# Performance work log

Hardware: AMD Instinct MI355X
Metric: run time of the kernel (lower is better)

Reference implementation:

```python
import jax, jax.numpy as jnp
import numpy as np

K = 8  # knn_k
EPS = 1e-5


def _grid_edges(H, W):
    # 4-connectivity grid edges, both directions. Returns (src, tgt) numpy int arrays.
    idx = np.arange(H * W).reshape(H, W)
    right_a, right_b = idx[:, :-1].ravel(), idx[:, 1:].ravel()
    down_a, down_b = idx[:-1, :].ravel(), idx[1:, :].ravel()
    src = np.concatenate([right_a, right_b, down_a, down_b])
    tgt = np.concatenate([right_b, right_a, down_b, down_a])
    return src.astype(np.int32), tgt.astype(np.int32)


def setup_inputs() -> dict:
    key = jax.random.key(0)
    k1, _ = jax.random.split(key)
    feature_map = jax.random.normal(k1, (16, 256, 48, 48), dtype=jnp.float32)
    gamma = jnp.ones((256,), jnp.float32)
    beta = jnp.zeros((256,), jnp.float32)
    return {"feature_map": feature_map, "gamma": gamma, "beta": beta}


def reference(feature_map, gamma, beta):
    B, C, H, W = feature_map.shape
    N = H * W
    # flatten_feature_map: [B,C,H,W] -> [B,N,C]
    nodes = feature_map.reshape(B, C, N).transpose(0, 2, 1)

    # static grid edges (4-connectivity)
    g_src_np, g_tgt_np = _grid_edges(H, W)
    g_src = jnp.asarray(g_src_np)
    g_tgt = jnp.asarray(g_tgt_np)

    # feature-space kNN per sample (cdist + topk); exclude self with large diag
    big_diag = jnp.eye(N, dtype=nodes.dtype) * 1e9

    def knn_idx(x):  # x: [N, C]
        sq = jnp.sum(x * x, axis=1)
        d2 = sq[:, None] + sq[None, :] - 2.0 * (x @ x.T) + big_diag
        _, idx = jax.lax.top_k(-d2, K)  # [N, K] nearest neighbors
        return idx

    knn_src = jax.vmap(knn_idx)(nodes).reshape(B, N * K)  # per-sample sources
    knn_tgt = jnp.repeat(jnp.arange(N, dtype=jnp.int32), K)  # static targets

    tgt_all = jnp.concatenate([g_tgt, knn_tgt])  # same for all samples
    n_edges = tgt_all.shape[0]
    ones = jnp.ones((n_edges,), nodes.dtype)

    def aggregate(x, k_src):  # mean over incoming edges (fallback path)
        src_all = jnp.concatenate([g_src, k_src.astype(jnp.int32)])
        agg = jax.ops.segment_sum(x[src_all], tgt_all, num_segments=N)
        cnt = jax.ops.segment_sum(ones, tgt_all, num_segments=N)
        return agg / jnp.clip(cnt, 1.0)[:, None]

    refined = jax.vmap(aggregate)(nodes, knn_src)  # [B, N, C]

    # residual + LayerNorm over channel dim
    y = refined + nodes
    mu = jnp.mean(y, axis=-1, keepdims=True)
    var = jnp.mean((y - mu) ** 2, axis=-1, keepdims=True)
    y = (y - mu) * jax.lax.rsqrt(var + EPS) * gamma + beta

    # unflatten: [B,N,C] -> [B,C,H,W]
    return y.transpose(0, 2, 1).reshape(B, C, H, W)
```

## Files before the change

### kernel.cpp

```cpp
#include <hip/hip_runtime.h>

#define B_   16
#define C_   256
#define H_   48
#define W_   48
#define N_   (H_ * W_)
#define KNN  8

#define NG   (N_ / 32)
#define NT   17
#define FRAG 512
#define MPRE 10
#define JSPLIT 2
#define NCAND (JSPLIT * MPRE)

typedef __attribute__((ext_vector_type(8)))  short bf16x8;
typedef __attribute__((ext_vector_type(8)))  unsigned short u16x8;
typedef __attribute__((ext_vector_type(16))) float f32x16;

__device__ __forceinline__ unsigned short f2bf(float f) {
    unsigned int u = __float_as_uint(f);
    u = (u + 0x7FFF + ((u >> 16) & 1)) >> 16;
    return (unsigned short)u;
}
__device__ __forceinline__ float bf2f(unsigned short h) {
    return __uint_as_float(((unsigned int)h) << 16);
}
__device__ __forceinline__ bool lex_lt(float v, int i, float bv, int bi) {
    return (v < bv) || (v == bv && i < bi);
}
__device__ __forceinline__ unsigned int f2sort(float f) {
    unsigned int u = __float_as_uint(f);
    return u ^ ((unsigned int)((int)u >> 31) | 0x80000000u);
}

__global__ __launch_bounds__(256) void k_transpose(const float* __restrict__ fm,
                                                   float* __restrict__ nodes,
                                                   unsigned short* __restrict__ Xf) {
    __shared__ float tile[32][33];
    int b  = blockIdx.z;
    int n0 = blockIdx.x * 32;
    int c0 = blockIdx.y * 32;
    int tx = threadIdx.x, ty = threadIdx.y;
    const float* src = fm + (size_t)b * C_ * N_;
    float* dst = nodes + (size_t)b * N_ * C_;
    #pragma unroll
    for (int cc = 0; cc < 32; cc += 8)
        tile[cc + ty][tx] = src[(size_t)(c0 + cc + ty) * N_ + n0 + tx];
    __syncthreads();
    #pragma unroll
    for (int nn = 0; nn < 32; nn += 8)
        dst[(size_t)(n0 + nn + ty) * C_ + c0 + tx] = tile[tx][nn + ty];

    int flat = ty * 32 + tx;
    int wv = flat >> 6, lane = flat & 63;
    if (wv < 2) {
        int t   = 2 * blockIdx.y + wv;
        int l31 = lane & 31, lh = lane >> 5;
        u16x8 o;
        #pragma unroll
        for (int e = 0; e < 8; ++e)
            o[e] = f2bf(tile[wv * 16 + lh * 8 + e][l31]);
        unsigned short* df = Xf + (((size_t)b * NG + blockIdx.x) * NT + t) * FRAG + lane * 8;
        *(u16x8*)df = o;
    }
}

__global__ __launch_bounds__(256) void k_sq(const float* __restrict__ fm,
                                            float* __restrict__ sq,
                                            unsigned short* __restrict__ Xf) {
    int b = blockIdx.y;
    int n = blockIdx.x * 256 + threadIdx.x;
    const float* src = fm + (size_t)b * C_ * N_ + n;
    float s = 0.f;
    for (int c = 0; c < C_; ++c) { float v = src[(size_t)c * N_]; s = fmaf(v, v, s); }
    sq[b * N_ + n] = s;

    float sh = -0.5f * s;
    unsigned short e1 = f2bf(sh);
    unsigned short e2 = f2bf(sh - bf2f(e1));
    int g = n >> 5, l = n & 31;
    unsigned short* df = Xf + (((size_t)b * NG + g) * NT + 16) * FRAG + l * 8;
    u16x8 o = (u16x8){0, 0, 0, 0, 0, 0, 0, 0};
    o[0] = e1; o[1] = e2;
    *(u16x8*)df = o;
    u16x8 z = (u16x8){0, 0, 0, 0, 0, 0, 0, 0};
    *(u16x8*)(df + 32 * 8) = z;
}

__global__ __launch_bounds__(256) void k_knn_mfma(const unsigned short* __restrict__ Xf,
                                                  int* __restrict__ pi_pre) {
    __shared__ unsigned int ms[2][32][2][2][MPRE];

    int b   = blockIdx.z;
    int i0  = blockIdx.x * 64;
    int js  = blockIdx.y;
    int tid = threadIdx.x;
    int wave = tid >> 6, lane = tid & 63;
    int wi = wave & 1, wj = wave >> 1;
    int l31 = lane & 31, lh = lane >> 5;

    const unsigned short* Xb = Xf + (size_t)b * NG * NT * FRAG;
    int gi = (i0 >> 5) + wi;

    bf16x8 bfr[16];
    const unsigned short* ibase = Xb + (size_t)gi * NT * FRAG + lane * 8;
    #pragma unroll
    for (int t = 0; t < 16; ++t) bfr[t] = *(const bf16x8*)(ibase + t * FRAG);
    short one = (lh == 0) ? (short)0x3F80 : (short)0;
    bf16x8 bc = (bf16x8){one, one, 0, 0, 0, 0, 0, 0};

    int I0 = i0 + wi * 32 + l31;

    unsigned int best[MPRE];
    #pragma unroll
    for (int q = 0; q < MPRE; ++q) best[q] = 0u;

    for (int jt = 0; jt < 18; ++jt) {
        int gj = js * (NG / JSPLIT) + jt * 2 + wj;
        const unsigned short* ab = Xb + (size_t)gj * NT * FRAG + lane * 8;

        f32x16 acc;
        #pragma unroll
        for (int r = 0; r < 16; ++r) acc[r] = 0.f;

        #pragma unroll
        for (int t = 0; t < 16; ++t) {
            bf16x8 af = *(const bf16x8*)(ab + t * FRAG);
            acc = __builtin_amdgcn_mfma_f32_32x32x16_bf16(af, bfr[t], acc, 0, 0, 0);
        }
        {
            bf16x8 af = *(const bf16x8*)(ab + 16 * FRAG);
            acc = __builtin_amdgcn_mfma_f32_32x32x16_bf16(af, bc, acc, 0, 0, 0);
        }

        int j0 = gj * 32;
        int idxbase = 4095 - j0 - 4 * lh;
        #pragma unroll
        for (int r = 0; r < 16; ++r) {
            int cr = (r & 3) + 8 * (r >> 2);
            int gjrow = j0 + cr + 4 * lh;
            unsigned int p = (f2sort(acc[r]) & 0xFFFFF000u) | (unsigned int)(idxbase - cr);
            p = (gjrow == I0) ? 0u : p;
            #pragma unroll
            for (int q = 0; q < MPRE; ++q) {
                unsigned int hi = p > best[q] ? p : best[q];
                unsigned int lo = p > best[q] ? best[q] : p;
                best[q] = hi; p = lo;
            }
        }
    }

    #pragma unroll
    for (int q = 0; q < MPRE; ++q) ms[wi][l31][wj][lh][q] = best[q];
    __syncthreads();
    if (tid < 64) {
        int mwi = tid >> 5, mcol = tid & 31;
        unsigned int mb[MPRE];
        #pragma unroll
        for (int q = 0; q < MPRE; ++q) mb[q] = 0u;
        for (int wjj = 0; wjj < 2; ++wjj)
            for (int hh = 0; hh < 2; ++hh)
                #pragma unroll
                for (int qq = 0; qq < MPRE; ++qq) {
                    unsigned int p = ms[mwi][mcol][wjj][hh][qq];
                    #pragma unroll
                    for (int q = 0; q < MPRE; ++q) {
                        unsigned int hi = p > mb[q] ? p : mb[q];
                        unsigned int lo = p > mb[q] ? mb[q] : p;
                        mb[q] = hi; p = lo;
                    }
                }
        int i_g = i0 + mwi * 32 + mcol;
        int* dst = pi_pre + (((size_t)b * N_ + i_g) * JSPLIT + js) * MPRE;
        #pragma unroll
        for (int q = 0; q < MPRE; ++q) dst[q] = 4095 - (int)(mb[q] & 0xFFFu);
    }
}

__global__ __launch_bounds__(256) void k_rerank(const float* __restrict__ nodes,
                                                const float* __restrict__ sq,
                                                const int* __restrict__ pi_pre,
                                                int* __restrict__ knn) {
    __shared__ float d2s[4][NCAND];
    __shared__ int   jss[4][NCAND];

    int wv   = threadIdx.x >> 6;
    int lane = threadIdx.x & 63;
    int row  = blockIdx.x * 4 + wv;
    int g = lane >> 4, m = lane & 15;
    int b = row / N_;
    const float* Xb = nodes + (size_t)b * N_ * C_;
    const float* xi = nodes + (size_t)row * C_;

    float4 xiv[4];
    #pragma unroll
    for (int p = 0; p < 4; ++p) xiv[p] = *(const float4*)&xi[p * 64 + m * 4];
    float sqi = sq[row];
    const int* cand = pi_pre + (size_t)row * NCAND;

    for (int it = 0; it < 5; ++it) {
        int c = it * 4 + g;
        int j = cand[c];
        bool valid = (unsigned)j < (unsigned)N_;
        int jc = valid ? j : 0;
        const float* xj = Xb + (size_t)jc * C_;
        float p = 0.f;
        #pragma unroll
        for (int pp = 0; pp < 4; ++pp) {
            float4 v = *(const float4*)&xj[pp * 64 + m * 4];
            p = fmaf(xiv[pp].x, v.x, p);
            p = fmaf(xiv[pp].y, v.y, p);
            p = fmaf(xiv[pp].z, v.z, p);
            p = fmaf(xiv[pp].w, v.w, p);
        }
        p += __shfl_xor(p, 1);
        p += __shfl_xor(p, 2);
        p += __shfl_xor(p, 4);
        p += __shfl_xor(p, 8);
        if (m == 0) {
            float d2 = valid ? (sqi + sq[b * N_ + jc] - 2.f * p) : 3.4e38f;
            d2s[wv][c] = d2;
            jss[wv][c] = valid ? j : 0x7fffffff;
        }
    }

    float bd[KNN]; int bj[KNN];
    #pragma unroll
    for (int q = 0; q < KNN; ++q) { bd[q] = 3.4e38f; bj[q] = 0x7fffffff; }
    for (int s = 0; s < NCAND; ++s) {
        float v = d2s[wv][s]; int jx = jss[wv][s];
        if (lex_lt(v, jx, bd[KNN - 1], bj[KNN - 1])) {
            float cv = v; int ci = jx;
            #pragma unroll
            for (int q = 0; q < KNN; ++q) {
                if (lex_lt(cv, ci, bd[q], bj[q])) {
                    float tv = bd[q]; bd[q] = cv; cv = tv;
                    int tx2 = bj[q]; bj[q] = ci; ci = tx2;
                }
            }
        }
    }
    if (lane == 0) {
        int* kr = knn + (size_t)row * KNN;
        #pragma unroll
        for (int q = 0; q < KNN; ++q) kr[q] = bj[q];
    }
}

__global__ __launch_bounds__(256) void k_agg_ln(const float* __restrict__ nodes,
                                                const int* __restrict__ knn,
                                                const float* __restrict__ gamma,
                                                const float* __restrict__ beta,
                                                float* __restrict__ out) {
    __shared__ float ytile[16][C_ + 1];

    int b   = blockIdx.y;
    int i0  = blockIdx.x * 16;
    int tid = threadIdx.x;
    int wv = tid >> 6, lane = tid & 63;
    const float* Xb = nodes + (size_t)b * N_ * C_;

    float4 g4 = *(const float4*)&gamma[lane * 4];
    float4 b4 = *(const float4*)&beta[lane * 4];

    for (int rr = 0; rr < 4; ++rr) {
        int ii = wv * 4 + rr;
        int i  = i0 + ii;
        int x_ = i % W_;
        int y_ = i / W_;
        float s0 = 0.f, s1 = 0.f, s2 = 0.f, s3 = 0.f;
        int cnt = KNN;

        #define ADDROW(J) { float4 v = *(const float4*)&Xb[(size_t)(J) * C_ + lane * 4]; \
                            s0 += v.x; s1 += v.y; s2 += v.z; s3 += v.w; }
        if (x_ > 0)      { ADDROW(i - 1);  cnt++; }
        if (x_ < W_ - 1) { ADDROW(i + 1);  cnt++; }
        if (y_ > 0)      { ADDROW(i - W_); cnt++; }
        if (y_ < H_ - 1) { ADDROW(i + W_); cnt++; }
        const int* kr = knn + ((size_t)b * N_ + i) * KNN;
        #pragma unroll
        for (int k = 0; k < KNN; ++k) ADDROW(kr[k]);
        #undef ADDROW

        float4 xi = *(const float4*)&Xb[(size_t)i * C_ + lane * 4];
        float ic = 1.f / (float)cnt;
        float y0 = s0 * ic + xi.x;
        float y1 = s1 * ic + xi.y;
        float y2 = s2 * ic + xi.z;
        float y3 = s3 * ic + xi.w;

        float rx = y0 + y1 + y2 + y3;
        float ry = y0 * y0 + y1 * y1 + y2 * y2 + y3 * y3;
        #pragma unroll
        for (int mm = 1; mm < 64; mm <<= 1) {
            rx += __shfl_xor(rx, mm);
            ry += __shfl_xor(ry, mm);
        }
        float mu  = rx * (1.f / C_);
        float var = ry * (1.f / C_) - mu * mu;
        float inv = rsqrtf(var + 1e-5f);

        ytile[ii][lane * 4 + 0] = (y0 - mu) * inv * g4.x + b4.x;
        ytile[ii][lane * 4 + 1] = (y1 - mu) * inv * g4.y + b4.y;
        ytile[ii][lane * 4 + 2] = (y2 - mu) * inv * g4.z + b4.z;
        ytile[ii][lane * 4 + 3] = (y3 - mu) * inv * g4.w + b4.w;
    }
    __syncthreads();

    float* op = out + (size_t)b * C_ * N_ + (size_t)tid * N_ + i0;
    float vv[16];
    #pragma unroll
    for (int ii = 0; ii < 16; ++ii) vv[ii] = ytile[ii][tid];
    #pragma unroll
    for (int q = 0; q < 4; ++q) {
        float4 w;
        w.x = vv[q * 4 + 0]; w.y = vv[q * 4 + 1];
        w.z = vv[q * 4 + 2]; w.w = vv[q * 4 + 3];
        *(float4*)&op[q * 4] = w;
    }
}

extern "C" void kernel_launch(void* const* d_in, const int* in_sizes, int n_in,
                              void* d_out, int out_size, void* d_ws, size_t ws_size,
                              hipStream_t stream) {
    const float* fm    = (const float*)d_in[0];
    const float* gamma = (const float*)d_in[1];
    const float* beta  = (const float*)d_in[2];
    float* out = (float*)d_out;

    char* ws = (char*)d_ws;
    size_t off = 0;
    float* nodes = (float*)(ws + off); off += (size_t)B_ * N_ * C_ * sizeof(float);
    float* sq    = (float*)(ws + off); off += (size_t)B_ * N_ * sizeof(float);
    int*   knn   = (int*)  (ws + off); off += (size_t)B_ * N_ * KNN * sizeof(int);
    unsigned short* Xf = (unsigned short*)(ws + off);
    off += (size_t)B_ * NG * NT * FRAG * sizeof(unsigned short);
    int* pi_pre = (int*)(ws + off);
    off += (size_t)B_ * N_ * NCAND * sizeof(int);

    k_transpose<<<dim3(N_ / 32, C_ / 32, B_), dim3(32, 8), 0, stream>>>(fm, nodes, Xf);
    k_sq<<<dim3(N_ / 256, B_), 256, 0, stream>>>(fm, sq, Xf);
    k_knn_mfma<<<dim3(N_ / 64, JSPLIT, B_), 256, 0, stream>>>(Xf, pi_pre);
    k_rerank<<<(B_ * N_) / 4, 256, 0, stream>>>(nodes, sq, pi_pre, knn);
    k_agg_ln<<<dim3(N_ / 16, B_), 256, 0, stream>>>(nodes, knn, gamma, beta, out);
}
```

Measured before the change: 384.6 us.

## Cover all j-columns per kNN block with 8 waves and swizzled block order

The kNN MFMA kernel no longer splits the j-range across two blocks. Each 512-thread block now uses 8 waves that together cover all 72 column groups, and the two lane halves merge their top-10 lists with a cross-lane shuffle before the shared-memory merge. The merge now keeps a top-20 per row instead of two independent top-10 lists. Block IDs are remapped with an XCD-style swizzle so blocks of the same sample land together, which may improve L2 reuse of the Xf fragments. In exchange, candidate selection becomes a global top-20 rather than per-half top-10s, and the serial 64-thread merge now runs over a 20-entry array, which is longer.

```diff
diff --git a/kernel.cpp b/kernel.cpp
--- a/kernel.cpp
+++ b/kernel.cpp
@@ -11,8 +11,7 @@
 #define NT   17
 #define FRAG 512
 #define MPRE 10
-#define JSPLIT 2
-#define NCAND (JSPLIT * MPRE)
+#define NCAND 20
 
 typedef __attribute__((ext_vector_type(8)))  short bf16x8;
 typedef __attribute__((ext_vector_type(8)))  unsigned short u16x8;
@@ -88,13 +87,15 @@
     *(u16x8*)(df + 32 * 8) = z;
 }
 
-__global__ __launch_bounds__(256) void k_knn_mfma(const unsigned short* __restrict__ Xf,
+__global__ __launch_bounds__(512) void k_knn_mfma(const unsigned short* __restrict__ Xf,
                                                   int* __restrict__ pi_pre) {
-    __shared__ unsigned int ms[2][32][2][2][MPRE];
-
-    int b   = blockIdx.z;
-    int i0  = blockIdx.x * 64;
-    int js  = blockIdx.y;
+    __shared__ unsigned int ms[2][4][32][MPRE];
+
+    int bid  = blockIdx.x;
+    int wgid = (bid & 7) * 72 + (bid >> 3);
+    int b    = wgid / 36;
+    int i0   = (wgid % 36) * 64;
+
     int tid = threadIdx.x;
     int wave = tid >> 6, lane = tid & 63;
     int wi = wave & 1, wj = wave >> 1;
@@ -117,7 +118,7 @@
     for (int q = 0; q < MPRE; ++q) best[q] = 0u;
 
     for (int jt = 0; jt < 18; ++jt) {
-        int gj = js * (NG / JSPLIT) + jt * 2 + wj;
+        int gj = jt * 4 + wj;
         const unsigned short* ab = Xb + (size_t)gj * NT * FRAG + lane * 8;
 
         f32x16 acc;
@@ -151,30 +152,49 @@
         }
     }
 
-    #pragma unroll
-    for (int q = 0; q < MPRE; ++q) ms[wi][l31][wj][lh][q] = best[q];
+    {
+        unsigned int part[MPRE];
+        #pragma unroll
+        for (int q = 0; q < MPRE; ++q)
+            part[q] = (unsigned int)__shfl_xor((int)best[q], 32);
+        #pragma unroll
+        for (int q = 0; q < MPRE; ++q) {
+            unsigned int p = part[q];
+            #pragma unroll
+            for (int s = 0; s < MPRE; ++s) {
+                unsigned int hi = p > best[s] ? p : best[s];
+                unsigned int lo = p > best[s] ? best[s] : p;
+                best[s] = hi; p = lo;
+            }
+        }
+    }
+    if (lh == 0) {
+        #pragma unroll
+        for (int q = 0; q < MPRE; ++q) ms[wi][wj][l31][q] = best[q];
+    }
     __syncthreads();
+
     if (tid < 64) {
         int mwi = tid >> 5, mcol = tid & 31;
-        unsigned int mb[MPRE];
-        #pragma unroll
-        for (int q = 0; q < MPRE; ++q) mb[q] = 0u;
-        for (int wjj = 0; wjj < 2; ++wjj)
-            for (int hh = 0; hh < 2; ++hh)
+        unsigned int mb[NCAND];
+        #pragma unroll
+        for (int q = 0; q < NCAND; ++q) mb[q] = 0u;
+        for (int wjj = 0; wjj < 4; ++wjj) {
+            #pragma unroll
+            for (int qq = 0; qq < MPRE; ++qq) {
+                unsigned int p = ms[mwi][wjj][mcol][qq];
                 #pragma unroll
-                for (int qq = 0; qq < MPRE; ++qq) {
-                    unsigned int p = ms[mwi][mcol][wjj][hh][qq];
-                    #pragma unroll
-                    for (int q = 0; q < MPRE; ++q) {
-                        unsigned int hi = p > mb[q] ? p : mb[q];
-                        unsigned int lo = p > mb[q] ? mb[q] : p;
-                        mb[q] = hi; p = lo;
-                    }
+                for (int q = 0; q < NCAND; ++q) {
+                    unsigned int hi = p > mb[q] ? p : mb[q];
+                    unsigned int lo = p > mb[q] ? mb[q] : p;
+                    mb[q] = hi; p = lo;
                 }
-        int i_g = i0 + mwi * 32 + mcol;
-        int* dst = pi_pre + (((size_t)b * N_ + i_g) * JSPLIT + js) * MPRE;
-        #pragma unroll
-        for (int q = 0; q < MPRE; ++q) dst[q] = 4095 - (int)(mb[q] & 0xFFFu);
+            }
+        }
+        int i_g = i0 + tid;
+        int* dst = pi_pre + ((size_t)b * N_ + i_g) * NCAND;
+        #pragma unroll
+        for (int q = 0; q < NCAND; ++q) dst[q] = 4095 - (int)(mb[q] & 0xFFFu);
     }
 }
 
@@ -341,7 +361,7 @@
 
     k_transpose<<<dim3(N_ / 32, C_ / 32, B_), dim3(32, 8), 0, stream>>>(fm, nodes, Xf);
     k_sq<<<dim3(N_ / 256, B_), 256, 0, stream>>>(fm, sq, Xf);
-    k_knn_mfma<<<dim3(N_ / 64, JSPLIT, B_), 256, 0, stream>>>(Xf, pi_pre);
+    k_knn_mfma<<<(B_ * N_) / 64, 512, 0, stream>>>(Xf, pi_pre);
     k_rerank<<<(B_ * N_) / 4, 256, 0, stream>>>(nodes, sq, pi_pre, knn);
     k_agg_ln<<<dim3(N_ / 16, B_), 256, 0, stream>>>(nodes, knn, gamma, beta, out);
 }
```

After: 345.9 us. 10.1% less time.
